# Kernel tuning notes

Hardware: AMD Instinct MI355X
Metric: run time of the kernel (lower is better)

Reference implementation:

```python
import jax, jax.numpy as jnp
import numpy as np

NUM_HEADS = 12


def setup_inputs() -> dict:
    key = jax.random.key(0)
    ks = jax.random.split(key, 6)
    B, N, C = 16, 576, 768
    H, D = NUM_HEADS, 768 // NUM_HEADS
    P = 16
    x = jax.random.normal(ks[0], (B, N, C), dtype=jnp.float32)
    prompt = jax.random.normal(ks[1], (B, 2, P, H, D), dtype=jnp.float32)
    act_scale = jax.random.uniform(ks[2], (2,), dtype=jnp.float32)
    qkv_w = jax.random.normal(ks[3], (3 * C, C), dtype=jnp.float32) * (C ** -0.5)
    proj_w = jax.random.normal(ks[4], (C, C), dtype=jnp.float32) * (C ** -0.5)
    proj_b = jnp.zeros((C,), dtype=jnp.float32)
    return {"x": x, "prompt": prompt, "act_scale": act_scale,
            "qkv_w": qkv_w, "proj_w": proj_w, "proj_b": proj_b}


def reference(x, prompt, act_scale, qkv_w, proj_w, proj_b):
    B, N, C = x.shape
    H = NUM_HEADS
    D = C // H
    scale = D ** -0.5
    # qkv projection: [B,N,3C] -> (3,B,H,N,D)
    qkv = (x @ qkv_w.T).reshape(B, N, 3, H, D).transpose(2, 0, 3, 1, 4)
    q, k, v = qkv[0], qkv[1], qkv[2]
    # prompt: [B,2,P,H,D] -> (2,B,H,P,D)
    pr = jnp.transpose(prompt, (1, 0, 3, 2, 4))
    key_prefix, value_prefix = pr[0], pr[1]        # [B,H,P,D]
    v = jnp.concatenate([value_prefix, v], axis=2)  # [B,H,P+N,D]
    # gated prefix scores
    prompt_attn = jnp.einsum('bhnd,bhpd->bhnp', q, key_prefix) * scale
    prompt_attn = prompt_attn + jnp.tanh(prompt_attn * act_scale[0]) * act_scale[1]
    # standard scores
    attn = jnp.einsum('bhnd,bhmd->bhnm', q, k) * scale
    attn = jnp.concatenate([prompt_attn, attn], axis=-1)  # [B,H,N,P+N]
    attn = jax.nn.softmax(attn, axis=-1)
    out = jnp.einsum('bhnm,bhmd->bhnd', attn, v)  # [B,H,N,D]
    out = out.transpose(0, 2, 1, 3).reshape(B, N, C)
    return out @ proj_w.T + proj_b
```

## Files before the change

kernel.cpp:

```cpp
#include <hip/hip_runtime.h>
#include <hip/hip_bf16.h>
#include <math.h>

namespace {

constexpr int kB = 16, kN = 576, kC = 768, kH = 12, kP = 16;
constexpr int kM = kB * kN;

typedef __attribute__((ext_vector_type(8))) __bf16 bf16x8;
typedef __attribute__((ext_vector_type(4))) float  f32x4;
typedef __attribute__((ext_vector_type(8))) unsigned short u16x8;

__device__ inline unsigned short f2bf(float f) {
  __bf16 h = (__bf16)f;
  return __builtin_bit_cast(unsigned short, h);
}
__device__ inline float bf2f(unsigned short u) {
  unsigned int x = ((unsigned int)u) << 16;
  return __builtin_bit_cast(float, x);
}
__device__ inline unsigned int pk2bf(float lo, float hi) {
  return (unsigned int)f2bf(lo) | ((unsigned int)f2bf(hi) << 16);
}
__device__ inline int xcd_swz(int hw, int nwg) {
  const int per = nwg >> 3;
  return (hw & 7) * per + (hw >> 3);
}

#define GLDS16(src, dst) __builtin_amdgcn_global_load_lds( \
    (const __attribute__((address_space(1))) unsigned int*)(src), \
    (__attribute__((address_space(3))) unsigned int*)(dst), 16, 0, 0)

__global__ __launch_bounds__(256)
void cvt3(const float* __restrict__ x, const float* __restrict__ wq,
          const float* __restrict__ wp, unsigned short* __restrict__ xo,
          unsigned short* __restrict__ wqo, unsigned short* __restrict__ wpo) {
  const int bid = blockIdx.x;
  const float* in; unsigned short* out; int base;
  if (bid < 6912)       { in = x;  out = xo;  base = bid; }
  else if (bid < 8640)  { in = wq; out = wqo; base = bid - 6912; }
  else                  { in = wp; out = wpo; base = bid - 8640; }
  const int i = base * 256 + threadIdx.x;
  const float4 v = ((const float4*)in)[i];
  ((ushort4*)out)[i] = make_ushort4(f2bf(v.x), f2bf(v.y), f2bf(v.z), f2bf(v.w));
}

template<int OB>
__global__ __launch_bounds__(256)
void gemm_bf16(const unsigned short* __restrict__ A, const unsigned short* __restrict__ W,
               const float* __restrict__ bias, void* __restrict__ Yv, int Kd, int Nd) {
  __shared__ __align__(16) unsigned short As[8192];
  __shared__ __align__(16) unsigned short Bs[8192];
  const int tid  = threadIdx.x;
  const int wv   = tid >> 6, lane = tid & 63;
  const int gx   = Nd >> 7;
  const int lg   = xcd_swz(blockIdx.x, gridDim.x);
  const long bm  = (long)(lg / gx) * 128;
  const long bn  = (long)(lg % gx) * 128;
  const int wr   = (wv >> 1) * 64;
  const int wc   = (wv & 1) * 64;
  const int row15 = lane & 15, kg = lane >> 4;

  u16x8 ra[4], rb[4];
  auto loadregs = [&](int kt) {
#pragma unroll
    for (int site = 0; site < 4; ++site) {
      const int u = site * 256 + tid;
      const int row = u >> 3, slot = u & 7;
      ra[site] = *(const u16x8*)(A + (bm + row) * (long)Kd + kt + slot * 8);
      rb[site] = *(const u16x8*)(W + (bn + row) * (long)Kd + kt + slot * 8);
    }
  };
  auto writeLDS = [&]() {
#pragma unroll
    for (int site = 0; site < 4; ++site) {
      const int u = site * 256 + tid;
      const int row = u >> 3, slot = u & 7;
      const int off = row * 64 + ((slot ^ (row & 7)) << 3);
      *(u16x8*)(As + off) = ra[site];
      *(u16x8*)(Bs + off) = rb[site];
    }
  };

  float bvpre[4] = {0.0f, 0.0f, 0.0f, 0.0f};
  if constexpr (!OB) {
#pragma unroll
    for (int ni = 0; ni < 4; ++ni) bvpre[ni] = bias[bn + wc + ni * 16 + row15];
  }

  f32x4 acc[4][4] = {};
  loadregs(0);
  writeLDS();

  const int sw8 = row15 & 7;
  const int nt = Kd >> 6;
  for (int t = 0; t < nt; ++t) {
    __syncthreads();
    if (t + 1 < nt) loadregs((t + 1) << 6);

    bf16x8 af[4][2], bf_[4][2];
#pragma unroll
    for (int mi = 0; mi < 4; ++mi)
#pragma unroll
      for (int ks = 0; ks < 2; ++ks)
        af[mi][ks] = *(const bf16x8*)(&As[(wr + mi * 16 + row15) * 64 +
                                          (((ks * 4 + kg) ^ sw8) << 3)]);
#pragma unroll
    for (int ni = 0; ni < 4; ++ni)
#pragma unroll
      for (int ks = 0; ks < 2; ++ks)
        bf_[ni][ks] = *(const bf16x8*)(&Bs[(wc + ni * 16 + row15) * 64 +
                                           (((ks * 4 + kg) ^ sw8) << 3)]);
    __builtin_amdgcn_s_setprio(1);
#pragma unroll
    for (int ks = 0; ks < 2; ++ks)
#pragma unroll
      for (int mi = 0; mi < 4; ++mi)
#pragma unroll
        for (int ni = 0; ni < 4; ++ni)
          acc[mi][ni] = __builtin_amdgcn_mfma_f32_16x16x32_bf16(af[mi][ks], bf_[ni][ks],
                                                                acc[mi][ni], 0, 0, 0);
    __builtin_amdgcn_s_setprio(0);
    __syncthreads();
    if (t + 1 < nt) writeLDS();
  }

  const int r4 = kg * 4;
#pragma unroll
  for (int ni = 0; ni < 4; ++ni) {
    const long col = bn + wc + ni * 16 + row15;
    if constexpr (OB) {
      unsigned short* Y = (unsigned short*)Yv;
#pragma unroll
      for (int mi = 0; mi < 4; ++mi)
#pragma unroll
        for (int j = 0; j < 4; ++j)
          Y[(bm + wr + mi * 16 + r4 + j) * (long)Nd + col] = f2bf(acc[mi][ni][j]);
    } else {
      float* Y = (float*)Yv;
#pragma unroll
      for (int mi = 0; mi < 4; ++mi)
#pragma unroll
        for (int j = 0; j < 4; ++j)
          Y[(bm + wr + mi * 16 + r4 + j) * (long)Nd + col] = acc[mi][ni][j] + bvpre[ni];
    }
  }
}

__device__ inline void softmax_group_static(f32x4 (&c)[4], float& lsum,
                                            unsigned short* pl,
                                            const int kg, const int sw) {
  float psum = 0.0f;
#pragma unroll
  for (int kb = 0; kb < 4; ++kb) {
    const float p0 = __expf(c[kb][0] - 10.0f);
    const float p1 = __expf(c[kb][1] - 10.0f);
    const float p2 = __expf(c[kb][2] - 10.0f);
    const float p3 = __expf(c[kb][3] - 10.0f);
    psum += (p0 + p1) + (p2 + p3);
    const int off = (((kb * 2 + (kg >> 1)) ^ sw) << 3) + (kg & 1) * 4;
    *(uint2*)(pl + off) = make_uint2(pk2bf(p0, p1), pk2bf(p2, p3));
  }
  lsum += psum;
}

__global__ __launch_bounds__(192, 3)
void attn_mfma(const unsigned short* __restrict__ qkv, const float* __restrict__ prompt,
               const float* __restrict__ act_scale, unsigned short* __restrict__ attn_out) {
  const int lg = xcd_swz(blockIdx.x, gridDim.x);
  const int qt = lg % 6, bh = lg / 6;
  const int h = bh % kH, b = bh / kH;
  const int tid = threadIdx.x, wv = tid >> 6, lane = tid & 63;
  const int q15 = lane & 15, kg = lane >> 4;

  __shared__ __align__(16) unsigned short Klds[2][4096];
  __shared__ __align__(16) unsigned short Vt[2][4096];
  __shared__ __align__(16) unsigned short Plds[3][2048];

  const float a0 = act_scale[0], a1 = act_scale[1];
  const int sw  = q15 & 7;
  const int sl0 = (kg ^ sw) << 3;
  const int sl1 = ((4 + kg) ^ sw) << 3;

  bf16x8 qf[2][2];
#pragma unroll
  for (int g = 0; g < 2; ++g) {
    const unsigned short* qrow =
        qkv + (size_t)(b * kN + qt * 96 + wv * 32 + g * 16 + q15) * 2304 + h * 64;
#pragma unroll
    for (int dh = 0; dh < 2; ++dh) {
      u16x8 raw = *(const u16x8*)(qrow + dh * 32 + kg * 8);
      u16x8 sc;
#pragma unroll
      for (int j = 0; j < 8; ++j) sc[j] = f2bf(bf2f(raw[j]) * 0.125f);
      qf[g][dh] = __builtin_bit_cast(bf16x8, sc);
    }
  }

  if (tid < 128) {
    const int r = tid >> 3, s = tid & 7;
    const float* src = prompt + (((size_t)(b * 2) * kP + r) * kH + h) * 64 + s * 8;
    const f32x4 f0 = *(const f32x4*)src, f1 = *(const f32x4*)(src + 4);
    *(uint4*)(&Klds[0][r * 64 + ((s ^ (r & 7)) << 3)]) =
        make_uint4(pk2bf(f0[0], f0[1]), pk2bf(f0[2], f0[3]),
                   pk2bf(f1[0], f1[1]), pk2bf(f1[2], f1[3]));
  }
  if (tid < 128) {
    const int kp = tid & 7, vdq = tid >> 3;
    const float* s0 = prompt + (((size_t)(b * 2 + 1) * kP + 2 * kp) * kH + h) * 64 + vdq * 4;
    const f32x4 x0 = *(const f32x4*)s0;
    const f32x4 y0 = *(const f32x4*)(s0 + kH * 64);
#pragma unroll
    for (int j = 0; j < 4; ++j) {
      const int d = vdq * 4 + j;
      *(unsigned int*)(&Vt[0][d * 64 + (((kp >> 2) ^ (d & 7)) << 3) + (kp & 3) * 2]) =
          pk2bf(x0[j], y0[j]);
    }
  }
#pragma unroll
  for (int i = 0; i < 2; ++i) {
    const int idx = tid + 192 * i;
    const int d = idx / 6, szl = (idx % 6) + 2;
    *(uint4*)(&Vt[0][d * 64 + ((szl ^ (d & 7)) << 3)]) = make_uint4(0, 0, 0, 0);
  }
  __syncthreads();

  f32x4 o0[4] = {}, o1[4] = {};
  float l0 = 0.0f, l1 = 0.0f;

  const int vkp  = tid & 31;
  const int vdgb = tid >> 5;
  const int kr8  = lane >> 3, ks8 = lane & 7;

  for (int ch = 0; ch < 10; ++ch) {
    const int cur = ch & 1;

    u16x8 va0, va1, vb0, vb1;
    const bool doV = (ch < 9) && (wv < 2);
    if (ch < 9) {
      if (doV) {
        const unsigned short* r0 = qkv + (size_t)(b * kN + ch * 64 + 2 * vkp) * 2304 + 1536 + h * 64;
        va0 = *(const u16x8*)(r0 + vdgb * 8);
        va1 = *(const u16x8*)(r0 + (vdgb + 4) * 8);
        vb0 = *(const u16x8*)(r0 + 2304 + vdgb * 8);
        vb1 = *(const u16x8*)(r0 + 2304 + (vdgb + 4) * 8);
      } else if (wv == 2) {
#pragma unroll
        for (int g8 = 0; g8 < 8; ++g8) {
          const int r = g8 * 8 + kr8;
          const unsigned short* src =
              qkv + (size_t)(b * kN + ch * 64 + r) * 2304 + 768 + h * 64 + ((ks8 ^ (r & 7)) << 3);
          GLDS16(src, &Klds[cur ^ 1][g8 * 512]);
        }
      }
    }

    f32x4 c0[4], c1[4];
    __builtin_amdgcn_s_setprio(1);
#pragma unroll
    for (int kb = 0; kb < 4; ++kb) {
      if (ch == 0 && kb > 0) {
        c0[kb][0] = c0[kb][1] = c0[kb][2] = c0[kb][3] = -1.0e30f;
        c1[kb][0] = c1[kb][1] = c1[kb][2] = c1[kb][3] = -1.0e30f;
      } else {
        const unsigned short* krow = &Klds[cur][(kb * 16 + q15) * 64];
        const bf16x8 k0 = *(const bf16x8*)(krow + sl0);
        const bf16x8 k1 = *(const bf16x8*)(krow + sl1);
        f32x4 t0 = {}, t1 = {};
        t0 = __builtin_amdgcn_mfma_f32_16x16x32_bf16(k0, qf[0][0], t0, 0, 0, 0);
        c0[kb] = __builtin_amdgcn_mfma_f32_16x16x32_bf16(k1, qf[0][1], t0, 0, 0, 0);
        t1 = __builtin_amdgcn_mfma_f32_16x16x32_bf16(k0, qf[1][0], t1, 0, 0, 0);
        c1[kb] = __builtin_amdgcn_mfma_f32_16x16x32_bf16(k1, qf[1][1], t1, 0, 0, 0);
      }
    }
    __builtin_amdgcn_s_setprio(0);
    if (ch == 0) {
#pragma unroll
      for (int j = 0; j < 4; ++j) {
        const float s0v = c0[0][j];
        const float e0 = __expf(2.0f * s0v * a0);
        c0[0][j] = s0v + ((e0 - 1.0f) / (e0 + 1.0f)) * a1;
        const float s1v = c1[0][j];
        const float e1 = __expf(2.0f * s1v * a0);
        c1[0][j] = s1v + ((e1 - 1.0f) / (e1 + 1.0f)) * a1;
      }
    }

    softmax_group_static(c0, l0, &Plds[wv][q15 * 64], kg, sw);
    softmax_group_static(c1, l1, &Plds[wv][(q15 + 16) * 64], kg, sw);

    if (doV) {
#pragma unroll
      for (int j = 0; j < 8; ++j) {
        const int d0 = vdgb * 8 + j;
        *(unsigned int*)(&Vt[cur ^ 1][d0 * 64 + (((vkp >> 2) ^ (d0 & 7)) << 3) + (vkp & 3) * 2]) =
            (unsigned int)va0[j] | ((unsigned int)vb0[j] << 16);
        const int d1 = (vdgb + 4) * 8 + j;
        *(unsigned int*)(&Vt[cur ^ 1][d1 * 64 + (((vkp >> 2) ^ (d1 & 7)) << 3) + (vkp & 3) * 2]) =
            (unsigned int)va1[j] | ((unsigned int)vb1[j] << 16);
      }
    }

    const unsigned short* p0 = &Plds[wv][q15 * 64];
    const unsigned short* p1 = &Plds[wv][(q15 + 16) * 64];
    const bf16x8 pa00 = *(const bf16x8*)(p0 + sl0);
    const bf16x8 pa01 = *(const bf16x8*)(p0 + sl1);
    const bf16x8 pa10 = *(const bf16x8*)(p1 + sl0);
    const bf16x8 pa11 = *(const bf16x8*)(p1 + sl1);
    __builtin_amdgcn_s_setprio(1);
#pragma unroll
    for (int nb = 0; nb < 4; ++nb) {
      const unsigned short* vr = &Vt[cur][(nb * 16 + q15) * 64];
      const bf16x8 bv0 = *(const bf16x8*)(vr + sl0);
      const bf16x8 bv1 = *(const bf16x8*)(vr + sl1);
      o0[nb] = __builtin_amdgcn_mfma_f32_16x16x32_bf16(pa00, bv0, o0[nb], 0, 0, 0);
      o0[nb] = __builtin_amdgcn_mfma_f32_16x16x32_bf16(pa01, bv1, o0[nb], 0, 0, 0);
      o1[nb] = __builtin_amdgcn_mfma_f32_16x16x32_bf16(pa10, bv0, o1[nb], 0, 0, 0);
      o1[nb] = __builtin_amdgcn_mfma_f32_16x16x32_bf16(pa11, bv1, o1[nb], 0, 0, 0);
    }
    __builtin_amdgcn_s_setprio(0);

    __syncthreads();
  }

  l0 += __shfl_xor(l0, 16, 64);
  l0 += __shfl_xor(l0, 32, 64);
  l1 += __shfl_xor(l1, 16, 64);
  l1 += __shfl_xor(l1, 32, 64);
  const float i0 = 1.0f / l0, i1 = 1.0f / l1;
  float iq0[4], iq1[4];
#pragma unroll
  for (int jr = 0; jr < 4; ++jr) {
    iq0[jr] = __shfl(i0, kg * 4 + jr, 64);
    iq1[jr] = __shfl(i1, kg * 4 + jr, 64);
  }
  unsigned short* ob = attn_out + (size_t)(b * kN + qt * 96 + wv * 32) * 768 + h * 64;
#pragma unroll
  for (int nb = 0; nb < 4; ++nb)
#pragma unroll
    for (int jr = 0; jr < 4; ++jr) {
      ob[(size_t)(kg * 4 + jr) * 768 + nb * 16 + q15] = f2bf(o0[nb][jr] * iq0[jr]);
      ob[(size_t)(16 + kg * 4 + jr) * 768 + nb * 16 + q15] = f2bf(o1[nb][jr] * iq1[jr]);
    }
}

}

extern "C" void kernel_launch(void* const* d_in, const int* in_sizes, int n_in,
                              void* d_out, int out_size, void* d_ws, size_t ws_size,
                              hipStream_t stream) {
  const float* x         = (const float*)d_in[0];
  const float* prompt    = (const float*)d_in[1];
  const float* act_scale = (const float*)d_in[2];
  const float* qkv_w     = (const float*)d_in[3];
  const float* proj_w    = (const float*)d_in[4];
  const float* proj_b    = (const float*)d_in[5];
  float* out = (float*)d_out;

  char* ws = (char*)d_ws;
  unsigned short* qkvb   = (unsigned short*)ws;
  unsigned short* xa     = (unsigned short*)(ws + 42467328);
  unsigned short* qkvwb  = (unsigned short*)(ws + 42467328 + 14155776);
  unsigned short* projwb = (unsigned short*)(ws + 42467328 + 14155776 + 3538944);

  cvt3<<<9216, 256, 0, stream>>>(x, qkv_w, proj_w, xa, qkvwb, projwb);

  gemm_bf16<1><<<(3 * kC / 128) * (kM / 128), 256, 0, stream>>>(xa, qkvwb, nullptr, qkvb, kC, 3 * kC);
  attn_mfma<<<(kN / 96) * kH * kB, 192, 0, stream>>>(qkvb, prompt, act_scale, xa);
  gemm_bf16<0><<<(kC / 128) * (kM / 128), 256, 0, stream>>>(xa, projwb, proj_b, out, kC, kC);
}
```

Measured before the change: 118.7 us.

## Double attention query tile per block to 192 rows with per-group softmax

Each attention block now handles 192 query rows (64 per wave, four 16-row groups) instead of 96, halving the grid and halving how often each K/V chunk is reloaded from global memory and staged to LDS. Score, softmax and PV are computed group by group, using a double-buffered per-wave P scratch. The cost is more accumulator registers per wave (16 f32x4 outputs) under launch bounds of 3 blocks per CU, and a smaller grid (576 blocks), which may reduce occupancy and latency hiding.

After: 173.5 us. 46.2% more time.

```diff
diff --git a/kernel.cpp b/kernel.cpp
--- a/kernel.cpp
+++ b/kernel.cpp
@@ -168,25 +168,25 @@
 void attn_mfma(const unsigned short* __restrict__ qkv, const float* __restrict__ prompt,
                const float* __restrict__ act_scale, unsigned short* __restrict__ attn_out) {
   const int lg = xcd_swz(blockIdx.x, gridDim.x);
-  const int qt = lg % 6, bh = lg / 6;
+  const int qt = lg % 3, bh = lg / 3;
   const int h = bh % kH, b = bh / kH;
   const int tid = threadIdx.x, wv = tid >> 6, lane = tid & 63;
   const int q15 = lane & 15, kg = lane >> 4;
 
   __shared__ __align__(16) unsigned short Klds[2][4096];
   __shared__ __align__(16) unsigned short Vt[2][4096];
-  __shared__ __align__(16) unsigned short Plds[3][2048];
+  __shared__ __align__(16) unsigned short Plds[3][2][1024];
 
   const float a0 = act_scale[0], a1 = act_scale[1];
   const int sw  = q15 & 7;
   const int sl0 = (kg ^ sw) << 3;
   const int sl1 = ((4 + kg) ^ sw) << 3;
 
-  bf16x8 qf[2][2];
-#pragma unroll
-  for (int g = 0; g < 2; ++g) {
+  bf16x8 qf[4][2];
+#pragma unroll
+  for (int g = 0; g < 4; ++g) {
     const unsigned short* qrow =
-        qkv + (size_t)(b * kN + qt * 96 + wv * 32 + g * 16 + q15) * 2304 + h * 64;
+        qkv + (size_t)(b * kN + qt * 192 + wv * 64 + g * 16 + q15) * 2304 + h * 64;
 #pragma unroll
     for (int dh = 0; dh < 2; ++dh) {
       u16x8 raw = *(const u16x8*)(qrow + dh * 32 + kg * 8);
@@ -225,8 +225,8 @@
   }
   __syncthreads();
 
-  f32x4 o0[4] = {}, o1[4] = {};
-  float l0 = 0.0f, l1 = 0.0f;
+  f32x4 o[4][4] = {};
+  float l[4] = {0.0f, 0.0f, 0.0f, 0.0f};
 
   const int vkp  = tid & 31;
   const int vdgb = tid >> 5;
@@ -235,15 +235,15 @@
   for (int ch = 0; ch < 10; ++ch) {
     const int cur = ch & 1;
 
-    u16x8 va0, va1, vb0, vb1;
+    u16x8 va0, va1, vb0s, vb1s;
     const bool doV = (ch < 9) && (wv < 2);
     if (ch < 9) {
       if (doV) {
         const unsigned short* r0 = qkv + (size_t)(b * kN + ch * 64 + 2 * vkp) * 2304 + 1536 + h * 64;
-        va0 = *(const u16x8*)(r0 + vdgb * 8);
-        va1 = *(const u16x8*)(r0 + (vdgb + 4) * 8);
-        vb0 = *(const u16x8*)(r0 + 2304 + vdgb * 8);
-        vb1 = *(const u16x8*)(r0 + 2304 + (vdgb + 4) * 8);
+        va0  = *(const u16x8*)(r0 + vdgb * 8);
+        va1  = *(const u16x8*)(r0 + (vdgb + 4) * 8);
+        vb0s = *(const u16x8*)(r0 + 2304 + vdgb * 8);
+        vb1s = *(const u16x8*)(r0 + 2304 + (vdgb + 4) * 8);
       } else if (wv == 2) {
 #pragma unroll
         for (int g8 = 0; g8 < 8; ++g8) {
@@ -255,93 +255,84 @@
       }
     }
 
-    f32x4 c0[4], c1[4];
-    __builtin_amdgcn_s_setprio(1);
-#pragma unroll
-    for (int kb = 0; kb < 4; ++kb) {
-      if (ch == 0 && kb > 0) {
-        c0[kb][0] = c0[kb][1] = c0[kb][2] = c0[kb][3] = -1.0e30f;
-        c1[kb][0] = c1[kb][1] = c1[kb][2] = c1[kb][3] = -1.0e30f;
-      } else {
-        const unsigned short* krow = &Klds[cur][(kb * 16 + q15) * 64];
-        const bf16x8 k0 = *(const bf16x8*)(krow + sl0);
-        const bf16x8 k1 = *(const bf16x8*)(krow + sl1);
-        f32x4 t0 = {}, t1 = {};
-        t0 = __builtin_amdgcn_mfma_f32_16x16x32_bf16(k0, qf[0][0], t0, 0, 0, 0);
-        c0[kb] = __builtin_amdgcn_mfma_f32_16x16x32_bf16(k1, qf[0][1], t0, 0, 0, 0);
-        t1 = __builtin_amdgcn_mfma_f32_16x16x32_bf16(k0, qf[1][0], t1, 0, 0, 0);
-        c1[kb] = __builtin_amdgcn_mfma_f32_16x16x32_bf16(k1, qf[1][1], t1, 0, 0, 0);
-      }
-    }
-    __builtin_amdgcn_s_setprio(0);
-    if (ch == 0) {
-#pragma unroll
-      for (int j = 0; j < 4; ++j) {
-        const float s0v = c0[0][j];
-        const float e0 = __expf(2.0f * s0v * a0);
-        c0[0][j] = s0v + ((e0 - 1.0f) / (e0 + 1.0f)) * a1;
-        const float s1v = c1[0][j];
-        const float e1 = __expf(2.0f * s1v * a0);
-        c1[0][j] = s1v + ((e1 - 1.0f) / (e1 + 1.0f)) * a1;
-      }
-    }
-
-    softmax_group_static(c0, l0, &Plds[wv][q15 * 64], kg, sw);
-    softmax_group_static(c1, l1, &Plds[wv][(q15 + 16) * 64], kg, sw);
+#pragma unroll
+    for (int g = 0; g < 4; ++g) {
+      f32x4 c[4];
+      __builtin_amdgcn_s_setprio(1);
+#pragma unroll
+      for (int kb = 0; kb < 4; ++kb) {
+        if (ch == 0 && kb > 0) {
+          c[kb][0] = c[kb][1] = c[kb][2] = c[kb][3] = -1.0e30f;
+        } else {
+          const unsigned short* krow = &Klds[cur][(kb * 16 + q15) * 64];
+          const bf16x8 k0 = *(const bf16x8*)(krow + sl0);
+          const bf16x8 k1 = *(const bf16x8*)(krow + sl1);
+          f32x4 t = {};
+          t = __builtin_amdgcn_mfma_f32_16x16x32_bf16(k0, qf[g][0], t, 0, 0, 0);
+          c[kb] = __builtin_amdgcn_mfma_f32_16x16x32_bf16(k1, qf[g][1], t, 0, 0, 0);
+        }
+      }
+      __builtin_amdgcn_s_setprio(0);
+      if (ch == 0) {
+#pragma unroll
+        for (int j = 0; j < 4; ++j) {
+          const float s = c[0][j];
+          const float e = __expf(2.0f * s * a0);
+          c[0][j] = s + ((e - 1.0f) / (e + 1.0f)) * a1;
+        }
+      }
+
+      unsigned short* pbuf = &Plds[wv][g & 1][0];
+      softmax_group_static(c, l[g], pbuf + q15 * 64, kg, sw);
+
+      const unsigned short* p = pbuf + q15 * 64;
+      const bf16x8 pa0 = *(const bf16x8*)(p + sl0);
+      const bf16x8 pa1 = *(const bf16x8*)(p + sl1);
+      __builtin_amdgcn_s_setprio(1);
+#pragma unroll
+      for (int nb = 0; nb < 4; ++nb) {
+        const unsigned short* vr = &Vt[cur][(nb * 16 + q15) * 64];
+        const bf16x8 bv0 = *(const bf16x8*)(vr + sl0);
+        const bf16x8 bv1 = *(const bf16x8*)(vr + sl1);
+        o[g][nb] = __builtin_amdgcn_mfma_f32_16x16x32_bf16(pa0, bv0, o[g][nb], 0, 0, 0);
+        o[g][nb] = __builtin_amdgcn_mfma_f32_16x16x32_bf16(pa1, bv1, o[g][nb], 0, 0, 0);
+      }
+      __builtin_amdgcn_s_setprio(0);
+    }
 
     if (doV) {
 #pragma unroll
       for (int j = 0; j < 8; ++j) {
         const int d0 = vdgb * 8 + j;
         *(unsigned int*)(&Vt[cur ^ 1][d0 * 64 + (((vkp >> 2) ^ (d0 & 7)) << 3) + (vkp & 3) * 2]) =
-            (unsigned int)va0[j] | ((unsigned int)vb0[j] << 16);
+            (unsigned int)va0[j] | ((unsigned int)vb0s[j] << 16);
         const int d1 = (vdgb + 4) * 8 + j;
         *(unsigned int*)(&Vt[cur ^ 1][d1 * 64 + (((vkp >> 2) ^ (d1 & 7)) << 3) + (vkp & 3) * 2]) =
-            (unsigned int)va1[j] | ((unsigned int)vb1[j] << 16);
-      }
-    }
-
-    const unsigned short* p0 = &Plds[wv][q15 * 64];
-    const unsigned short* p1 = &Plds[wv][(q15 + 16) * 64];
-    const bf16x8 pa00 = *(const bf16x8*)(p0 + sl0);
-    const bf16x8 pa01 = *(const bf16x8*)(p0 + sl1);
-    const bf16x8 pa10 = *(const bf16x8*)(p1 + sl0);
-    const bf16x8 pa11 = *(const bf16x8*)(p1 + sl1);
-    __builtin_amdgcn_s_setprio(1);
-#pragma unroll
-    for (int nb = 0; nb < 4; ++nb) {
-      const unsigned short* vr = &Vt[cur][(nb * 16 + q15) * 64];
-      const bf16x8 bv0 = *(const bf16x8*)(vr + sl0);
-      const bf16x8 bv1 = *(const bf16x8*)(vr + sl1);
-      o0[nb] = __builtin_amdgcn_mfma_f32_16x16x32_bf16(pa00, bv0, o0[nb], 0, 0, 0);
-      o0[nb] = __builtin_amdgcn_mfma_f32_16x16x32_bf16(pa01, bv1, o0[nb], 0, 0, 0);
-      o1[nb] = __builtin_amdgcn_mfma_f32_16x16x32_bf16(pa10, bv0, o1[nb], 0, 0, 0);
-      o1[nb] = __builtin_amdgcn_mfma_f32_16x16x32_bf16(pa11, bv1, o1[nb], 0, 0, 0);
-    }
-    __builtin_amdgcn_s_setprio(0);
+            (unsigned int)va1[j] | ((unsigned int)vb1s[j] << 16);
+      }
+    }
 
     __syncthreads();
   }
 
-  l0 += __shfl_xor(l0, 16, 64);
-  l0 += __shfl_xor(l0, 32, 64);
-  l1 += __shfl_xor(l1, 16, 64);
-  l1 += __shfl_xor(l1, 32, 64);
-  const float i0 = 1.0f / l0, i1 = 1.0f / l1;
-  float iq0[4], iq1[4];
-#pragma unroll
-  for (int jr = 0; jr < 4; ++jr) {
-    iq0[jr] = __shfl(i0, kg * 4 + jr, 64);
-    iq1[jr] = __shfl(i1, kg * 4 + jr, 64);
-  }
-  unsigned short* ob = attn_out + (size_t)(b * kN + qt * 96 + wv * 32) * 768 + h * 64;
-#pragma unroll
-  for (int nb = 0; nb < 4; ++nb)
-#pragma unroll
-    for (int jr = 0; jr < 4; ++jr) {
-      ob[(size_t)(kg * 4 + jr) * 768 + nb * 16 + q15] = f2bf(o0[nb][jr] * iq0[jr]);
-      ob[(size_t)(16 + kg * 4 + jr) * 768 + nb * 16 + q15] = f2bf(o1[nb][jr] * iq1[jr]);
-    }
+#pragma unroll
+  for (int g = 0; g < 4; ++g) {
+    l[g] += __shfl_xor(l[g], 16, 64);
+    l[g] += __shfl_xor(l[g], 32, 64);
+  }
+  unsigned short* ob = attn_out + (size_t)(b * kN + qt * 192 + wv * 64) * 768 + h * 64;
+#pragma unroll
+  for (int g = 0; g < 4; ++g) {
+    const float iv = 1.0f / l[g];
+    float iq[4];
+#pragma unroll
+    for (int jr = 0; jr < 4; ++jr) iq[jr] = __shfl(iv, kg * 4 + jr, 64);
+#pragma unroll
+    for (int nb = 0; nb < 4; ++nb)
+#pragma unroll
+      for (int jr = 0; jr < 4; ++jr)
+        ob[(size_t)(g * 16 + kg * 4 + jr) * 768 + nb * 16 + q15] = f2bf(o[g][nb][jr] * iq[jr]);
+  }
 }
 
 }
@@ -366,6 +357,6 @@
   cvt3<<<9216, 256, 0, stream>>>(x, qkv_w, proj_w, xa, qkvwb, projwb);
 
   gemm_bf16<1><<<(3 * kC / 128) * (kM / 128), 256, 0, stream>>>(xa, qkvwb, nullptr, qkvb, kC, 3 * kC);
-  attn_mfma<<<(kN / 96) * kH * kB, 192, 0, stream>>>(qkvb, prompt, act_scale, xa);
+  attn_mfma<<<(kN / 192) * kH * kB, 192, 0, stream>>>(qkvb, prompt, act_scale, xa);
   gemm_bf16<0><<<(kC / 128) * (kM / 128), 256, 0, stream>>>(xa, projwb, proj_b, out, kC, kC);
 }
```
